# Kernel optimization log

Measured on AMD Instinct MI355X. Metric: run time of the kernel, lower is better.

## Reference

```python
import jax, jax.numpy as jnp
import numpy as np

B, S, I, H = 32, 512, 512, 512


def _lstm_dir(x_seq, Wih, Whh, bih, bhh, reverse):
    """Run a PyTorch-style LSTMCell over time. x_seq: [S, B, I]."""
    bsz = x_seq.shape[1]
    hid = Whh.shape[1]
    h0 = jnp.zeros((bsz, hid), x_seq.dtype)
    c0 = jnp.zeros((bsz, hid), x_seq.dtype)
    b = bih + bhh

    def step(carry, x_t):
        h, c = carry
        g = x_t @ Wih.T + h @ Whh.T + b           # [B, 4H]
        i_g, f_g, g_g, o_g = jnp.split(g, 4, axis=-1)
        c = jax.nn.sigmoid(f_g) * c + jax.nn.sigmoid(i_g) * jnp.tanh(g_g)
        h = jax.nn.sigmoid(o_g) * jnp.tanh(c)
        return (h, c), h

    (hN, cN), hs = jax.lax.scan(step, (h0, c0), x_seq, reverse=reverse)
    # with reverse=True, hs[t] is aligned with x_seq[t] (matches ht_b[::-1])
    return hs, hN, cN


def setup_inputs() -> dict:
    key = jax.random.key(0)
    ks = jax.random.split(key, 9)
    bound = 1.0 / np.sqrt(H)
    u = lambda k, shp: jax.random.uniform(k, shp, jnp.float32, -bound, bound)
    return {
        "X": jax.random.normal(ks[0], (B, S, I), jnp.float32),
        "Wih_f": u(ks[1], (4 * H, I)),
        "Whh_f": u(ks[2], (4 * H, H)),
        "bih_f": u(ks[3], (4 * H,)),
        "bhh_f": u(ks[4], (4 * H,)),
        "Wih_b": u(ks[5], (4 * H, I)),
        "Whh_b": u(ks[6], (4 * H, H)),
        "bih_b": u(ks[7], (4 * H,)),
        "bhh_b": u(ks[8], (4 * H,)),
    }


def reference(X, Wih_f, Whh_f, bih_f, bhh_f, Wih_b, Whh_b, bih_b, bhh_b):
    x_seq = jnp.transpose(X, (1, 0, 2))  # [S, B, I]
    hs_f, hN_f, cN_f = _lstm_dir(x_seq, Wih_f, Whh_f, bih_f, bhh_f, False)
    hs_b, hN_b, cN_b = _lstm_dir(x_seq, Wih_b, Whh_b, bih_b, bhh_b, True)
    # ht: [B, S, 2H]
    ht = jnp.transpose(jnp.concatenate([hs_f, hs_b], axis=-1), (1, 0, 2))
    stacked_h = jnp.stack([hN_f, hN_b])  # [2, B, H] (forward final, backward final)
    stacked_c = jnp.stack([cN_f, cN_b])
    return ht, (stacked_h, stacked_c)
```

## Files before the change

### kernel.cpp

```cpp
#include <hip/hip_runtime.h>
#include <hip/hip_bf16.h>

#define BSZ 32
#define SSZ 512
#define ISZ 512
#define HSZ 512
#define PW  32
#define XB_OFF   0ull
#define HEX_OFF  (16ull << 20)
#define CTR_OFF  (HEX_OFF + (128ull << 10))

typedef __attribute__((ext_vector_type(8)))  short short8;
typedef __attribute__((ext_vector_type(4)))  float f32x4;
typedef __attribute__((ext_vector_type(4)))  unsigned short us4;
typedef __attribute__((ext_vector_type(4)))  int i32x4;

__device__ __forceinline__ unsigned short f2bf(float f) {
    union { float f; unsigned u; } v; v.f = f;
    unsigned r = v.u + 0x7fffu + ((v.u >> 16) & 1u);
    return (unsigned short)(r >> 16);
}

__device__ __forceinline__ float sigf(float x) { return 1.0f / (1.0f + __expf(-x)); }
__device__ __forceinline__ float tanhfast(float x) {
    float a = fabsf(x);
    float e = __expf(-2.0f * a);
    float t = (1.0f - e) / (1.0f + e);
    return x < 0.0f ? -t : t;
}

__device__ __forceinline__ void dma16(const unsigned short* g, unsigned short* l) {
    __builtin_amdgcn_global_load_lds((const __attribute__((address_space(1))) unsigned int*)(g),
                                     (__attribute__((address_space(3))) unsigned int*)(l), 16, 0, 0);
}

__global__ void k_xpose(const float* __restrict__ X, unsigned short* __restrict__ Xb) {
    int idx = blockIdx.x * 256 + threadIdx.x;
    int i4 = idx & 127;
    int t  = (idx >> 7) & 511;
    int b  = idx >> 16;
    float4 v = reinterpret_cast<const float4*>(X)[idx];
    us4 o = { f2bf(v.x), f2bf(v.y), f2bf(v.z), f2bf(v.w) };
    *reinterpret_cast<us4*>(Xb + (size_t)t * 16384 + (size_t)(i4 >> 1) * 256 + b * 8 + (i4 & 1) * 4) = o;
}

__launch_bounds__(256, 1)
__global__ void k_bilstm(const float* __restrict__ Wih_f, const float* __restrict__ Whh_f,
                         const float* __restrict__ bih_f, const float* __restrict__ bhh_f,
                         const float* __restrict__ Wih_b, const float* __restrict__ Whh_b,
                         const float* __restrict__ bih_b, const float* __restrict__ bhh_b,
                         const unsigned short* __restrict__ Xb,
                         unsigned short* h_ex, unsigned* flags, float* __restrict__ out)
{
    const int tid = threadIdx.x;
    const int grp = blockIdx.x & 7;
    if (grp >= 2) return;
    const int dir  = grp;
    const int p    = blockIdx.x >> 3;
    const int wv   = tid >> 6;
    const int ln   = tid & 63;
    const int kh   = wv >> 1;
    const int half = wv & 1;
    const int q    = ln >> 4;
    const int m15  = ln & 15;

    unsigned* tab = flags + 4096;
    {
        unsigned xcc;
        asm volatile("s_getreg_b32 %0, hwreg(20, 0, 32)" : "=s"(xcc));
        if (tid == 0)
            __hip_atomic_store(tab + dir * 32 + p, (xcc & 7u) + 1u,
                               __ATOMIC_RELAXED, __HIP_MEMORY_SCOPE_AGENT);
    }

    const float* Wsel = kh ? (dir ? Whh_b : Whh_f) : (dir ? Wih_b : Wih_f);
    const float* bi   = dir ? bih_b : bih_f;
    const float* bh   = dir ? bhh_b : bhh_f;

    __shared__ float gates[4][32][67];
    __shared__ float cst[32][16];
    __shared__ float outbuf[2][32][16];
    __shared__ float bias[64];
    __shared__ int   mode_sh;
    __shared__ __align__(16) unsigned short xstage[2][2][8192];

    short8 breg[8][4];
#pragma unroll
    for (int ks = 0; ks < 8; ++ks) {
#pragma unroll
        for (int g = 0; g < 4; ++g) {
            const float* wr = Wsel + (size_t)(g * 512 + p * 16 + m15) * 512
                                   + half * 256 + ks * 32 + q * 8;
            short8 bb;
#pragma unroll
            for (int j = 0; j < 8; ++j) bb[j] = (short)f2bf(wr[j]);
            breg[ks][g] = bb;
        }
    }

    if (tid < 64) {
        int c = tid;
        int gr = (c >> 4) * 512 + p * 16 + (c & 15);
        bias[c] = bi[gr] + bh[gr];
    }
    for (int i = tid; i < 512; i += 256) ((float*)cst)[i] = 0.0f;

    if (tid < 64) {
        const unsigned* tp = tab + dir * 32 + (tid & 31);
        unsigned v;
        do { v = __hip_atomic_load(tp, __ATOMIC_RELAXED, __HIP_MEMORY_SCOPE_AGENT); } while (v == 0u);
        unsigned ref = __shfl(v, 0);
        int same = (__ballot(v == ref) == ~0ull) ? 1 : 0;
        if (tid == 0) mode_sh = same;
    }
    __syncthreads();
    const int fast = mode_sh;

    unsigned* flg = flags + (size_t)dir * 2048;
    unsigned short* hexd = h_ex + (size_t)dir * 2 * 16384;

    if (kh == 0) {
        int t0 = dir ? 511 : 0;
        const unsigned short* src = Xb + (size_t)t0 * 16384 + half * 8192 + ln * 8;
        unsigned short* lb = &xstage[half][0][0];
#pragma unroll
        for (int j = 0; j < 16; ++j) dma16(src + j * 512, lb + j * 512);
    }

    int agent_poll = 0;

    for (int s = 0; s < 512; ++s) {
        f32x4 acc[4][2];
#pragma unroll
        for (int g = 0; g < 4; ++g) { acc[g][0] = {0.f,0.f,0.f,0.f}; acc[g][1] = {0.f,0.f,0.f,0.f}; }

        if (kh == 0) {
            asm volatile("s_waitcnt vmcnt(0)" ::: "memory");
            __builtin_amdgcn_sched_barrier(0);
            const unsigned short* xs = &xstage[half][s & 1][0];
#pragma unroll
            for (int ks = 0; ks < 8; ++ks) {
                const unsigned short* ap = xs + (ks * 4 + q) * 256 + m15 * 8;
                short8 a0 = *reinterpret_cast<const short8*>(ap);
                short8 a1 = *reinterpret_cast<const short8*>(ap + 128);
#pragma unroll
                for (int g = 0; g < 4; ++g) {
                    acc[g][0] = __builtin_amdgcn_mfma_f32_16x16x32_bf16(a0, breg[ks][g], acc[g][0], 0, 0, 0);
                    acc[g][1] = __builtin_amdgcn_mfma_f32_16x16x32_bf16(a1, breg[ks][g], acc[g][1], 0, 0, 0);
                }
            }
            if (s > 0) {
                int pt = dir ? (512 - s) : (s - 1);
                int L = half * 64 + ln; int b = L >> 2; int qd = L & 3;
                f32x4 hvv = *reinterpret_cast<const f32x4*>(&outbuf[(s - 1) & 1][b][qd * 4]);
                *reinterpret_cast<f32x4*>(&out[(size_t)b * 524288 + (size_t)pt * 1024
                                               + dir * 512 + p * 16 + qd * 4]) = hvv;
            }
        } else if (fast) {
            if (s > 0) {
                const unsigned* fp = flg + (ln & 31);
                if (!agent_poll) {
                    int spins = 0;
                    for (;;) {
                        unsigned v;
                        asm volatile("global_load_dword %0, %1, off sc0\n\t"
                                     "s_waitcnt vmcnt(0)"
                                     : "=&v"(v) : "v"(fp) : "memory");
                        if (__ballot((int)(v >= (unsigned)s)) == ~0ull) break;
                        if (++spins > 20000) { agent_poll = 1; break; }
                    }
                }
                if (agent_poll) {
                    for (;;) {
                        unsigned v = __hip_atomic_load(fp, __ATOMIC_RELAXED, __HIP_MEMORY_SCOPE_AGENT);
                        if (__ballot((int)(v >= (unsigned)s)) == ~0ull) break;
                    }
                }
                asm volatile("" ::: "memory");
            }
            const unsigned short* ab = hexd + (size_t)((s + 1) & 1) * 16384 + half * 8192;
            i32x4 A0[8], A1[8];
#pragma unroll
            for (int ks = 0; ks < 8; ++ks) {
                const unsigned short* ap = ab + (ks * 4 + q) * 256 + m15 * 8;
                asm volatile("global_load_dwordx4 %0, %2, off sc0\n\t"
                             "global_load_dwordx4 %1, %3, off sc0"
                             : "=&v"(A0[ks]), "=&v"(A1[ks])
                             : "v"(ap), "v"(ap + 128) : "memory");
            }
#pragma unroll
            for (int ks = 0; ks < 8; ++ks) {
                asm volatile("s_waitcnt vmcnt(%0)" :: "n"(14 - 2 * ks) : "memory");
                __builtin_amdgcn_sched_barrier(0);
                short8 a0 = __builtin_bit_cast(short8, A0[ks]);
                short8 a1 = __builtin_bit_cast(short8, A1[ks]);
#pragma unroll
                for (int g = 0; g < 4; ++g) {
                    acc[g][0] = __builtin_amdgcn_mfma_f32_16x16x32_bf16(a0, breg[ks][g], acc[g][0], 0, 0, 0);
                    acc[g][1] = __builtin_amdgcn_mfma_f32_16x16x32_bf16(a1, breg[ks][g], acc[g][1], 0, 0, 0);
                }
            }
        } else {
            if (s > 0) {
                const unsigned* fp = flg + (ln & 31);
                for (;;) {
                    unsigned v = __hip_atomic_load(fp, __ATOMIC_RELAXED, __HIP_MEMORY_SCOPE_AGENT);
                    if (__ballot((int)(v >= (unsigned)s)) == ~0ull) break;
                }
                asm volatile("" ::: "memory");
            }
            const unsigned* abase = reinterpret_cast<const unsigned*>(hexd + (size_t)((s + 1) & 1) * 16384);
#pragma unroll
            for (int ks = 0; ks < 8; ++ks) {
                const unsigned* ap = abase + ((half * 32 + ks * 4 + q) * 256 + m15 * 8) / 2;
                union { short8 s8; unsigned u[4]; } ua0, ua1;
#pragma unroll
                for (int w = 0; w < 4; ++w) {
                    ua0.u[w] = __hip_atomic_load(ap + w,      __ATOMIC_RELAXED, __HIP_MEMORY_SCOPE_AGENT);
                    ua1.u[w] = __hip_atomic_load(ap + 64 + w, __ATOMIC_RELAXED, __HIP_MEMORY_SCOPE_AGENT);
                }
#pragma unroll
                for (int g = 0; g < 4; ++g) {
                    acc[g][0] = __builtin_amdgcn_mfma_f32_16x16x32_bf16(ua0.s8, breg[ks][g], acc[g][0], 0, 0, 0);
                    acc[g][1] = __builtin_amdgcn_mfma_f32_16x16x32_bf16(ua1.s8, breg[ks][g], acc[g][1], 0, 0, 0);
                }
            }
        }

#pragma unroll
        for (int g = 0; g < 4; ++g)
#pragma unroll
            for (int r = 0; r < 4; ++r) {
                gates[wv][q * 4 + r][g * 16 + m15]      = acc[g][0][r];
                gates[wv][16 + q * 4 + r][g * 16 + m15] = acc[g][1][r];
            }
        asm volatile("s_waitcnt lgkmcnt(0)" ::: "memory");
        __builtin_amdgcn_s_barrier();

        {
            int b  = tid >> 3;
            int j0 = (tid & 7) * 2;
            float hv01[2];
#pragma unroll
            for (int u = 0; u < 2; ++u) {
                int j = j0 + u;
                float ig = gates[0][b][j]      + gates[1][b][j]      + gates[2][b][j]      + gates[3][b][j]      + bias[j];
                float fg = gates[0][b][16 + j] + gates[1][b][16 + j] + gates[2][b][16 + j] + gates[3][b][16 + j] + bias[16 + j];
                float gg = gates[0][b][32 + j] + gates[1][b][32 + j] + gates[2][b][32 + j] + gates[3][b][32 + j] + bias[32 + j];
                float og = gates[0][b][48 + j] + gates[1][b][48 + j] + gates[2][b][48 + j] + gates[3][b][48 + j] + bias[48 + j];
                float cn = sigf(fg) * cst[b][j] + sigf(ig) * tanhfast(gg);
                cst[b][j] = cn;
                hv01[u] = sigf(og) * tanhfast(cn);
            }
            *reinterpret_cast<float2*>(&outbuf[s & 1][b][j0]) = make_float2(hv01[0], hv01[1]);
            int hc0 = p * 16 + j0;
            unsigned pk = (unsigned)f2bf(hv01[0]) | ((unsigned)f2bf(hv01[1]) << 16);
            unsigned* dst = reinterpret_cast<unsigned*>(
                hexd + (size_t)(s & 1) * 16384 + (size_t)(hc0 >> 3) * 256 + b * 8 + (hc0 & 7));
            if (fast) {
                asm volatile("global_store_dword %0, %1, off sc0" :: "v"(dst), "v"(pk) : "memory");
            } else {
                __hip_atomic_store(dst, pk, __ATOMIC_RELAXED, __HIP_MEMORY_SCOPE_AGENT);
            }
        }

        if (kh == 0 && s < 511) {
            int tn = dir ? (510 - s) : (s + 1);
            const unsigned short* src = Xb + (size_t)tn * 16384 + half * 8192 + ln * 8;
            unsigned short* lb = &xstage[half][(s + 1) & 1][0];
#pragma unroll
            for (int j = 0; j < 16; ++j) dma16(src + j * 512, lb + j * 512);
        }

        if (kh == 0) {
            if (s < 511) { asm volatile("s_waitcnt vmcnt(16)" ::: "memory"); }
            else         { asm volatile("s_waitcnt vmcnt(0)"  ::: "memory"); }
        } else {
            asm volatile("s_waitcnt vmcnt(0)" ::: "memory");
        }
        asm volatile("s_waitcnt lgkmcnt(0)" ::: "memory");
        __builtin_amdgcn_s_barrier();
        if (tid == 0) {
            if (fast) {
                unsigned sv = (unsigned)(s + 1);
                asm volatile("global_store_dword %0, %1, off sc0" :: "v"(flg + p), "v"(sv) : "memory");
            } else {
                __hip_atomic_store(flg + p, (unsigned)(s + 1), __ATOMIC_RELAXED, __HIP_MEMORY_SCOPE_AGENT);
            }
        }
    }

    if (kh == 0) {
        int L = half * 64 + ln; int b = L >> 2; int qd = L & 3;
        int tl = dir ? 0 : 511;
        f32x4 hvv = *reinterpret_cast<const f32x4*>(&outbuf[1][b][qd * 4]);
        *reinterpret_cast<f32x4*>(&out[(size_t)b * 524288 + (size_t)tl * 1024
                                       + dir * 512 + p * 16 + qd * 4]) = hvv;
        *reinterpret_cast<f32x4*>(&out[16777216 + dir * 16384 + b * 512 + p * 16 + qd * 4]) = hvv;
        f32x4 cvv = *reinterpret_cast<const f32x4*>(&cst[b][qd * 4]);
        *reinterpret_cast<f32x4*>(&out[16777216 + 32768 + dir * 16384 + b * 512 + p * 16 + qd * 4]) = cvv;
    }
}

extern "C" void kernel_launch(void* const* d_in, const int* in_sizes, int n_in,
                              void* d_out, int out_size, void* d_ws, size_t ws_size,
                              hipStream_t stream) {
    const float* X     = (const float*)d_in[0];
    const float* Wih_f = (const float*)d_in[1];
    const float* Whh_f = (const float*)d_in[2];
    const float* bih_f = (const float*)d_in[3];
    const float* bhh_f = (const float*)d_in[4];
    const float* Wih_b = (const float*)d_in[5];
    const float* Whh_b = (const float*)d_in[6];
    const float* bih_b = (const float*)d_in[7];
    const float* bhh_b = (const float*)d_in[8];
    float* out = (float*)d_out;

    unsigned short* Xb   = (unsigned short*)((char*)d_ws + XB_OFF);
    unsigned short* h_ex = (unsigned short*)((char*)d_ws + HEX_OFF);
    unsigned*       flg  = (unsigned*)((char*)d_ws + CTR_OFF);

    hipMemsetAsync((char*)d_ws + HEX_OFF, 0, (128ull + 64ull) << 10, stream);
    k_xpose<<<8192, 256, 0, stream>>>(X, Xb);
    k_bilstm<<<256, 256, 0, stream>>>(Wih_f, Whh_f, bih_f, bhh_f,
                                      Wih_b, Whh_b, bih_b, bhh_b,
                                      Xb, h_ex, flg, out);
}
```

Measured before the change: 2.998 ms.

## Precompute input projection three steps ahead in a shared-memory FIFO

```diff
diff --git a/kernel.cpp b/kernel.cpp
--- a/kernel.cpp
+++ b/kernel.cpp
@@ -5,7 +5,6 @@
 #define SSZ 512
 #define ISZ 512
 #define HSZ 512
-#define PW  32
 #define XB_OFF   0ull
 #define HEX_OFF  (16ull << 20)
 #define CTR_OFF  (HEX_OFF + (128ull << 10))
@@ -27,11 +26,6 @@
     float e = __expf(-2.0f * a);
     float t = (1.0f - e) / (1.0f + e);
     return x < 0.0f ? -t : t;
-}
-
-__device__ __forceinline__ void dma16(const unsigned short* g, unsigned short* l) {
-    __builtin_amdgcn_global_load_lds((const __attribute__((address_space(1))) unsigned int*)(g),
-                                     (__attribute__((address_space(3))) unsigned int*)(l), 16, 0, 0);
 }
 
 __global__ void k_xpose(const float* __restrict__ X, unsigned short* __restrict__ Xb) {
@@ -59,8 +53,8 @@
     const int p    = blockIdx.x >> 3;
     const int wv   = tid >> 6;
     const int ln   = tid & 63;
-    const int kh   = wv >> 1;
-    const int half = wv & 1;
+    const int isx  = (wv < 2);
+    const int nt   = wv & 1;
     const int q    = ln >> 4;
     const int m15  = ln & 15;
 
@@ -73,29 +67,43 @@
                                __ATOMIC_RELAXED, __HIP_MEMORY_SCOPE_AGENT);
     }
 
-    const float* Wsel = kh ? (dir ? Whh_b : Whh_f) : (dir ? Wih_b : Wih_f);
-    const float* bi   = dir ? bih_b : bih_f;
-    const float* bh   = dir ? bhh_b : bhh_f;
-
-    __shared__ float gates[4][32][67];
+    const float* Wih = dir ? Wih_b : Wih_f;
+    const float* Whh = dir ? Whh_b : Whh_f;
+    const float* bi  = dir ? bih_b : bih_f;
+    const float* bh  = dir ? bhh_b : bhh_f;
+
+    __shared__ float gates[2][32][67];
+    __shared__ float fifo[4][32][67];
     __shared__ float cst[32][16];
     __shared__ float outbuf[2][32][16];
     __shared__ float bias[64];
     __shared__ int   mode_sh;
-    __shared__ __align__(16) unsigned short xstage[2][2][8192];
-
-    short8 breg[8][4];
-#pragma unroll
-    for (int ks = 0; ks < 8; ++ks) {
-#pragma unroll
-        for (int g = 0; g < 4; ++g) {
-            const float* wr = Wsel + (size_t)(g * 512 + p * 16 + m15) * 512
-                                   + half * 256 + ks * 32 + q * 8;
-            short8 bb;
-#pragma unroll
-            for (int j = 0; j < 8; ++j) bb[j] = (short)f2bf(wr[j]);
-            breg[ks][g] = bb;
-        }
+
+    short8 breg[32];
+    if (isx) {
+#pragma unroll
+        for (int ks = 0; ks < 16; ++ks)
+#pragma unroll
+            for (int gg = 0; gg < 2; ++gg) {
+                const float* wr = Wih + (size_t)((nt * 2 + gg) * 512 + p * 16 + m15) * 512
+                                      + ks * 32 + q * 8;
+                short8 bb;
+#pragma unroll
+                for (int j = 0; j < 8; ++j) bb[j] = (short)f2bf(wr[j]);
+                breg[ks * 2 + gg] = bb;
+            }
+    } else {
+#pragma unroll
+        for (int ks = 0; ks < 8; ++ks)
+#pragma unroll
+            for (int g = 0; g < 4; ++g) {
+                const float* wr = Whh + (size_t)(g * 512 + p * 16 + m15) * 512
+                                      + nt * 256 + ks * 32 + q * 8;
+                short8 bb;
+#pragma unroll
+                for (int j = 0; j < 8; ++j) bb[j] = (short)f2bf(wr[j]);
+                breg[ks * 4 + g] = bb;
+            }
     }
 
     if (tid < 64) {
@@ -119,135 +127,147 @@
     unsigned* flg = flags + (size_t)dir * 2048;
     unsigned short* hexd = h_ex + (size_t)dir * 2 * 16384;
 
-    if (kh == 0) {
-        int t0 = dir ? 511 : 0;
-        const unsigned short* src = Xb + (size_t)t0 * 16384 + half * 8192 + ln * 8;
-        unsigned short* lb = &xstage[half][0][0];
-#pragma unroll
-        for (int j = 0; j < 16; ++j) dma16(src + j * 512, lb + j * 512);
-    }
+    auto produce = [&](int sp) {
+        int t = dir ? (511 - sp) : sp;
+        const unsigned short* abase = Xb + (size_t)t * 16384;
+        f32x4 xa[2][2];
+#pragma unroll
+        for (int gg = 0; gg < 2; ++gg) { xa[gg][0] = {0.f,0.f,0.f,0.f}; xa[gg][1] = {0.f,0.f,0.f,0.f}; }
+#pragma unroll
+        for (int ks = 0; ks < 16; ++ks) {
+            const unsigned short* ap = abase + (ks * 4 + q) * 256 + m15 * 8;
+            short8 a0 = *reinterpret_cast<const short8*>(ap);
+            short8 a1 = *reinterpret_cast<const short8*>(ap + 128);
+#pragma unroll
+            for (int gg = 0; gg < 2; ++gg) {
+                xa[gg][0] = __builtin_amdgcn_mfma_f32_16x16x32_bf16(a0, breg[ks * 2 + gg], xa[gg][0], 0, 0, 0);
+                xa[gg][1] = __builtin_amdgcn_mfma_f32_16x16x32_bf16(a1, breg[ks * 2 + gg], xa[gg][1], 0, 0, 0);
+            }
+        }
+        float (*fp)[67] = fifo[sp & 3];
+#pragma unroll
+        for (int gg = 0; gg < 2; ++gg)
+#pragma unroll
+            for (int r = 0; r < 4; ++r) {
+                fp[q * 4 + r][(nt * 2 + gg) * 16 + m15]      = xa[gg][0][r];
+                fp[16 + q * 4 + r][(nt * 2 + gg) * 16 + m15] = xa[gg][1][r];
+            }
+    };
+
+    if (isx) { produce(0); produce(1); produce(2); }
 
     int agent_poll = 0;
 
     for (int s = 0; s < 512; ++s) {
-        f32x4 acc[4][2];
-#pragma unroll
-        for (int g = 0; g < 4; ++g) { acc[g][0] = {0.f,0.f,0.f,0.f}; acc[g][1] = {0.f,0.f,0.f,0.f}; }
-
-        if (kh == 0) {
-            asm volatile("s_waitcnt vmcnt(0)" ::: "memory");
-            __builtin_amdgcn_sched_barrier(0);
-            const unsigned short* xs = &xstage[half][s & 1][0];
-#pragma unroll
-            for (int ks = 0; ks < 8; ++ks) {
-                const unsigned short* ap = xs + (ks * 4 + q) * 256 + m15 * 8;
-                short8 a0 = *reinterpret_cast<const short8*>(ap);
-                short8 a1 = *reinterpret_cast<const short8*>(ap + 128);
-#pragma unroll
-                for (int g = 0; g < 4; ++g) {
-                    acc[g][0] = __builtin_amdgcn_mfma_f32_16x16x32_bf16(a0, breg[ks][g], acc[g][0], 0, 0, 0);
-                    acc[g][1] = __builtin_amdgcn_mfma_f32_16x16x32_bf16(a1, breg[ks][g], acc[g][1], 0, 0, 0);
-                }
-            }
+        if (isx) {
             if (s > 0) {
                 int pt = dir ? (512 - s) : (s - 1);
-                int L = half * 64 + ln; int b = L >> 2; int qd = L & 3;
+                int L = nt * 64 + ln; int b = L >> 2; int qd = L & 3;
                 f32x4 hvv = *reinterpret_cast<const f32x4*>(&outbuf[(s - 1) & 1][b][qd * 4]);
                 *reinterpret_cast<f32x4*>(&out[(size_t)b * 524288 + (size_t)pt * 1024
                                                + dir * 512 + p * 16 + qd * 4]) = hvv;
             }
-        } else if (fast) {
-            if (s > 0) {
-                const unsigned* fp = flg + (ln & 31);
-                if (!agent_poll) {
-                    int spins = 0;
-                    for (;;) {
-                        unsigned v;
-                        asm volatile("global_load_dword %0, %1, off sc0\n\t"
-                                     "s_waitcnt vmcnt(0)"
-                                     : "=&v"(v) : "v"(fp) : "memory");
-                        if (__ballot((int)(v >= (unsigned)s)) == ~0ull) break;
-                        if (++spins > 20000) { agent_poll = 1; break; }
-                    }
-                }
-                if (agent_poll) {
+            if (s + 3 < 512) produce(s + 3);
+        } else {
+            f32x4 acc[4][2];
+#pragma unroll
+            for (int g = 0; g < 4; ++g) { acc[g][0] = {0.f,0.f,0.f,0.f}; acc[g][1] = {0.f,0.f,0.f,0.f}; }
+
+            if (fast) {
+                if (s > 0) {
+                    const unsigned* fp = flg + (ln & 31);
+                    if (!agent_poll) {
+                        int spins = 0;
+                        for (;;) {
+                            unsigned v;
+                            asm volatile("global_load_dword %0, %1, off sc0\n\t"
+                                         "s_waitcnt vmcnt(0)"
+                                         : "=&v"(v) : "v"(fp) : "memory");
+                            if (__ballot((int)(v >= (unsigned)s)) == ~0ull) break;
+                            if (++spins > 20000) { agent_poll = 1; break; }
+                        }
+                    }
+                    if (agent_poll) {
+                        for (;;) {
+                            unsigned v = __hip_atomic_load(fp, __ATOMIC_RELAXED, __HIP_MEMORY_SCOPE_AGENT);
+                            if (__ballot((int)(v >= (unsigned)s)) == ~0ull) break;
+                        }
+                    }
+                    asm volatile("" ::: "memory");
+                }
+                const unsigned short* ab = hexd + (size_t)((s + 1) & 1) * 16384 + nt * 8192;
+                i32x4 A0[8], A1[8];
+#pragma unroll
+                for (int ks = 0; ks < 8; ++ks) {
+                    const unsigned short* ap = ab + (ks * 4 + q) * 256 + m15 * 8;
+                    asm volatile("global_load_dwordx4 %0, %2, off sc0\n\t"
+                                 "global_load_dwordx4 %1, %3, off sc0"
+                                 : "=&v"(A0[ks]), "=&v"(A1[ks])
+                                 : "v"(ap), "v"(ap + 128) : "memory");
+                }
+#pragma unroll
+                for (int ks = 0; ks < 8; ++ks) {
+                    asm volatile("s_waitcnt vmcnt(%0)" :: "n"(14 - 2 * ks) : "memory");
+                    __builtin_amdgcn_sched_barrier(0);
+                    short8 a0 = __builtin_bit_cast(short8, A0[ks]);
+                    short8 a1 = __builtin_bit_cast(short8, A1[ks]);
+#pragma unroll
+                    for (int g = 0; g < 4; ++g) {
+                        acc[g][0] = __builtin_amdgcn_mfma_f32_16x16x32_bf16(a0, breg[ks * 4 + g], acc[g][0], 0, 0, 0);
+                        acc[g][1] = __builtin_amdgcn_mfma_f32_16x16x32_bf16(a1, breg[ks * 4 + g], acc[g][1], 0, 0, 0);
+                    }
+                }
+            } else {
+                if (s > 0) {
+                    const unsigned* fp = flg + (ln & 31);
                     for (;;) {
                         unsigned v = __hip_atomic_load(fp, __ATOMIC_RELAXED, __HIP_MEMORY_SCOPE_AGENT);
                         if (__ballot((int)(v >= (unsigned)s)) == ~0ull) break;
                     }
-                }
-                asm volatile("" ::: "memory");
-            }
-            const unsigned short* ab = hexd + (size_t)((s + 1) & 1) * 16384 + half * 8192;
-            i32x4 A0[8], A1[8];
-#pragma unroll
-            for (int ks = 0; ks < 8; ++ks) {
-                const unsigned short* ap = ab + (ks * 4 + q) * 256 + m15 * 8;
-                asm volatile("global_load_dwordx4 %0, %2, off sc0\n\t"
-                             "global_load_dwordx4 %1, %3, off sc0"
-                             : "=&v"(A0[ks]), "=&v"(A1[ks])
-                             : "v"(ap), "v"(ap + 128) : "memory");
-            }
-#pragma unroll
-            for (int ks = 0; ks < 8; ++ks) {
-                asm volatile("s_waitcnt vmcnt(%0)" :: "n"(14 - 2 * ks) : "memory");
-                __builtin_amdgcn_sched_barrier(0);
-                short8 a0 = __builtin_bit_cast(short8, A0[ks]);
-                short8 a1 = __builtin_bit_cast(short8, A1[ks]);
-#pragma unroll
-                for (int g = 0; g < 4; ++g) {
-                    acc[g][0] = __builtin_amdgcn_mfma_f32_16x16x32_bf16(a0, breg[ks][g], acc[g][0], 0, 0, 0);
-                    acc[g][1] = __builtin_amdgcn_mfma_f32_16x16x32_bf16(a1, breg[ks][g], acc[g][1], 0, 0, 0);
-                }
-            }
-        } else {
-            if (s > 0) {
-                const unsigned* fp = flg + (ln & 31);
-                for (;;) {
-                    unsigned v = __hip_atomic_load(fp, __ATOMIC_RELAXED, __HIP_MEMORY_SCOPE_AGENT);
-                    if (__ballot((int)(v >= (unsigned)s)) == ~0ull) break;
-                }
-                asm volatile("" ::: "memory");
-            }
-            const unsigned* abase = reinterpret_cast<const unsigned*>(hexd + (size_t)((s + 1) & 1) * 16384);
-#pragma unroll
-            for (int ks = 0; ks < 8; ++ks) {
-                const unsigned* ap = abase + ((half * 32 + ks * 4 + q) * 256 + m15 * 8) / 2;
-                union { short8 s8; unsigned u[4]; } ua0, ua1;
-#pragma unroll
-                for (int w = 0; w < 4; ++w) {
-                    ua0.u[w] = __hip_atomic_load(ap + w,      __ATOMIC_RELAXED, __HIP_MEMORY_SCOPE_AGENT);
-                    ua1.u[w] = __hip_atomic_load(ap + 64 + w, __ATOMIC_RELAXED, __HIP_MEMORY_SCOPE_AGENT);
-                }
-#pragma unroll
-                for (int g = 0; g < 4; ++g) {
-                    acc[g][0] = __builtin_amdgcn_mfma_f32_16x16x32_bf16(ua0.s8, breg[ks][g], acc[g][0], 0, 0, 0);
-                    acc[g][1] = __builtin_amdgcn_mfma_f32_16x16x32_bf16(ua1.s8, breg[ks][g], acc[g][1], 0, 0, 0);
-                }
-            }
+                    asm volatile("" ::: "memory");
+                }
+                const unsigned* abase = reinterpret_cast<const unsigned*>(hexd + (size_t)((s + 1) & 1) * 16384);
+#pragma unroll
+                for (int ks = 0; ks < 8; ++ks) {
+                    const unsigned* ap = abase + ((nt * 32 + ks * 4 + q) * 256 + m15 * 8) / 2;
+                    union { short8 s8; unsigned u[4]; } ua0, ua1;
+#pragma unroll
+                    for (int w = 0; w < 4; ++w) {
+                        ua0.u[w] = __hip_atomic_load(ap + w,      __ATOMIC_RELAXED, __HIP_MEMORY_SCOPE_AGENT);
+                        ua1.u[w] = __hip_atomic_load(ap + 64 + w, __ATOMIC_RELAXED, __HIP_MEMORY_SCOPE_AGENT);
+                    }
+#pragma unroll
+                    for (int g = 0; g < 4; ++g) {
+                        acc[g][0] = __builtin_amdgcn_mfma_f32_16x16x32_bf16(ua0.s8, breg[ks * 4 + g], acc[g][0], 0, 0, 0);
+                        acc[g][1] = __builtin_amdgcn_mfma_f32_16x16x32_bf16(ua1.s8, breg[ks * 4 + g], acc[g][1], 0, 0, 0);
+                    }
+                }
+            }
+
+#pragma unroll
+            for (int g = 0; g < 4; ++g)
+#pragma unroll
+                for (int r = 0; r < 4; ++r) {
+                    gates[nt][q * 4 + r][g * 16 + m15]      = acc[g][0][r];
+                    gates[nt][16 + q * 4 + r][g * 16 + m15] = acc[g][1][r];
+                }
         }
 
-#pragma unroll
-        for (int g = 0; g < 4; ++g)
-#pragma unroll
-            for (int r = 0; r < 4; ++r) {
-                gates[wv][q * 4 + r][g * 16 + m15]      = acc[g][0][r];
-                gates[wv][16 + q * 4 + r][g * 16 + m15] = acc[g][1][r];
-            }
         asm volatile("s_waitcnt lgkmcnt(0)" ::: "memory");
         __builtin_amdgcn_s_barrier();
 
         {
+            const float (*xp)[67] = fifo[s & 3];
             int b  = tid >> 3;
             int j0 = (tid & 7) * 2;
             float hv01[2];
 #pragma unroll
             for (int u = 0; u < 2; ++u) {
                 int j = j0 + u;
-                float ig = gates[0][b][j]      + gates[1][b][j]      + gates[2][b][j]      + gates[3][b][j]      + bias[j];
-                float fg = gates[0][b][16 + j] + gates[1][b][16 + j] + gates[2][b][16 + j] + gates[3][b][16 + j] + bias[16 + j];
-                float gg = gates[0][b][32 + j] + gates[1][b][32 + j] + gates[2][b][32 + j] + gates[3][b][32 + j] + bias[32 + j];
-                float og = gates[0][b][48 + j] + gates[1][b][48 + j] + gates[2][b][48 + j] + gates[3][b][48 + j] + bias[48 + j];
+                float ig = gates[0][b][j]      + gates[1][b][j]      + xp[b][j]      + bias[j];
+                float fg = gates[0][b][16 + j] + gates[1][b][16 + j] + xp[b][16 + j] + bias[16 + j];
+                float gg = gates[0][b][32 + j] + gates[1][b][32 + j] + xp[b][32 + j] + bias[32 + j];
+                float og = gates[0][b][48 + j] + gates[1][b][48 + j] + xp[b][48 + j] + bias[48 + j];
                 float cn = sigf(fg) * cst[b][j] + sigf(ig) * tanhfast(gg);
                 cst[b][j] = cn;
                 hv01[u] = sigf(og) * tanhfast(cn);
@@ -264,20 +284,7 @@
             }
         }
 
-        if (kh == 0 && s < 511) {
-            int tn = dir ? (510 - s) : (s + 1);
-            const unsigned short* src = Xb + (size_t)tn * 16384 + half * 8192 + ln * 8;
-            unsigned short* lb = &xstage[half][(s + 1) & 1][0];
-#pragma unroll
-            for (int j = 0; j < 16; ++j) dma16(src + j * 512, lb + j * 512);
-        }
-
-        if (kh == 0) {
-            if (s < 511) { asm volatile("s_waitcnt vmcnt(16)" ::: "memory"); }
-            else         { asm volatile("s_waitcnt vmcnt(0)"  ::: "memory"); }
-        } else {
-            asm volatile("s_waitcnt vmcnt(0)" ::: "memory");
-        }
+        asm volatile("s_waitcnt vmcnt(0)" ::: "memory");
         asm volatile("s_waitcnt lgkmcnt(0)" ::: "memory");
         __builtin_amdgcn_s_barrier();
         if (tid == 0) {
@@ -290,8 +297,8 @@
         }
     }
 
-    if (kh == 0) {
-        int L = half * 64 + ln; int b = L >> 2; int qd = L & 3;
+    if (isx) {
+        int L = nt * 64 + ln; int b = L >> 2; int qd = L & 3;
         int tl = dir ? 0 : 511;
         f32x4 hvv = *reinterpret_cast<const f32x4*>(&outbuf[1][b][qd * 4]);
         *reinterpret_cast<f32x4*>(&out[(size_t)b * 524288 + (size_t)tl * 1024
```

After: 4.230 ms. 41.1% more time.
